# Performance work log

Hardware: AMD Instinct MI355X
Metric: run time of the kernel (lower is better)

Reference implementation:

```python
import jax, jax.numpy as jnp
import numpy as np

N_HEAD = 16
HEAD_DIM = 64

def setup_inputs() -> dict:
    key = jax.random.key(0)
    k1, k2, k3 = jax.random.split(key, 3)
    B, S, D = 4, 2048, 1024
    x = jax.random.normal(k1, (B, S, D), dtype=jnp.float32)
    mask = jnp.tril(jnp.ones((S, S), dtype=bool))[None, None]  # (1,1,S,S) causal
    w_attn = jax.random.normal(k2, (D, 3 * D), dtype=jnp.float32) * (1.0 / np.sqrt(D))
    b_attn = jnp.zeros((3 * D,), dtype=jnp.float32)
    w_proj = jax.random.normal(k3, (D, D), dtype=jnp.float32) * (1.0 / np.sqrt(D))
    b_proj = jnp.zeros((D,), dtype=jnp.float32)
    return {"x": x, "mask": mask, "w_attn": w_attn, "b_attn": b_attn,
            "w_proj": w_proj, "b_proj": b_proj}

def reference(x, mask, w_attn, b_attn, w_proj, b_proj):
    B, S, D = x.shape
    H, hd = N_HEAD, HEAD_DIM
    qkv = x @ w_attn + b_attn                      # (B,S,3D)
    q, k, v = jnp.split(qkv, 3, axis=-1)
    q = q.reshape(B, S, H, hd).transpose(0, 2, 1, 3)  # (B,H,S,hd)
    k = k.reshape(B, S, H, hd).transpose(0, 2, 1, 3)
    v = v.reshape(B, S, H, hd).transpose(0, 2, 1, 3)
    scores = jnp.einsum('bhqd,bhkd->bhqk', q, k) / jnp.sqrt(jnp.float32(hd))
    scores = jnp.where(mask, scores, jnp.float32(-1e10))
    weights = jax.nn.softmax(scores, axis=-1)      # dropout is identity (deterministic=True)
    attn = jnp.einsum('bhqk,bhkd->bhqd', weights, v)
    attn = attn.transpose(0, 2, 1, 3).reshape(B, S, D)
    return attn @ w_proj + b_proj
```

## Files before the change

### kernel.cpp

```cpp
#include <hip/hip_runtime.h>
#include <hip/hip_bf16.h>
#include <stdint.h>


typedef uint16_t u16;
typedef __bf16 bf16x8 __attribute__((ext_vector_type(8)));
typedef __bf16 bf16x4 __attribute__((ext_vector_type(4)));
typedef float f32x4 __attribute__((ext_vector_type(4)));

#define S_LEN 2048
#define DMODEL 1024
#define NHEAD 16
#define HDIM 64
#define MTOT 8192
#define NQKV 3072

__device__ __forceinline__ u16 f2bf(float f) {
    union { float f; uint32_t u; } v; v.f = f;
    uint32_t u = v.u;
    return (u16)((u + 0x7fffu + ((u >> 16) & 1u)) >> 16);
}

__device__ __forceinline__ void async_load16(const void* g, void* l) {
    __builtin_amdgcn_global_load_lds(
        (__attribute__((address_space(1))) void*)g,
        (__attribute__((address_space(3))) void*)l,
        16, 0, 0);
}

__global__ void convert_x_kernel(const float4* __restrict__ in, ushort4* __restrict__ out, int n4) {
    int i = blockIdx.x * 256 + threadIdx.x;
    if (i < n4) {
        float4 f = in[i];
        ushort4 o;
        o.x = f2bf(f.x); o.y = f2bf(f.y); o.z = f2bf(f.z); o.w = f2bf(f.w);
        out[i] = o;
    }
}

__global__ void transpose_bf16_kernel(const float* __restrict__ in, u16* __restrict__ out, int R, int C) {
    __shared__ float tile[64][65];
    int r0 = blockIdx.y * 64, c0 = blockIdx.x * 64;
    #pragma unroll
    for (int i = 0; i < 16; ++i) {
        int idx = threadIdx.x + i * 256;
        int r = idx >> 6, c = idx & 63;
        tile[r][c] = in[(size_t)(r0 + r) * C + c0 + c];
    }
    __syncthreads();
    #pragma unroll
    for (int i = 0; i < 16; ++i) {
        int idx = threadIdx.x + i * 256;
        int c = idx >> 6, r = idx & 63;
        out[(size_t)(c0 + c) * R + r0 + r] = f2bf(tile[r][c]);
    }
}

__global__ void transpose_v_kernel(const u16* __restrict__ qkv, u16* __restrict__ vt) {
    __shared__ u16 tile[64 * 66];
    const int tid = threadIdx.x;
    const int stile = blockIdx.x, bh = blockIdx.y;
    const int b = bh >> 4, h = bh & 15;
    const u16* src = qkv + ((size_t)b * S_LEN + stile * 64) * NQKV + 2 * DMODEL + h * HDIM;
    #pragma unroll
    for (int it = 0; it < 2; ++it) {
        int item = it * 256 + tid;
        int s = item >> 3, d0 = (item & 7) * 8;
        bf16x8 v = *(const bf16x8*)(src + (size_t)s * NQKV + d0);
        const u16* vu = (const u16*)&v;
        #pragma unroll
        for (int j = 0; j < 8; ++j) tile[(d0 + j) * 66 + s] = vu[j];
    }
    __syncthreads();
    #pragma unroll
    for (int it = 0; it < 2; ++it) {
        int item = it * 256 + tid;
        int d = item >> 3, s0 = (item & 7) * 8;
        union { u16 u[8]; uint4 v; } pk;
        #pragma unroll
        for (int j = 0; j < 8; ++j) pk.u[j] = tile[d * 66 + s0 + j];
        *(uint4*)(vt + ((size_t)bh * 64 + d) * S_LEN + stile * 64 + s0) = pk.v;
    }
}

template<bool OUT_BF16>
__global__ __launch_bounds__(256, 2) void gemm_bt(
    const u16* __restrict__ A, const u16* __restrict__ Bt,
    const float* __restrict__ bias, void* __restrict__ C,
    int M, int N, int K)
{
    __shared__ __attribute__((aligned(16))) u16 As[128 * 32];
    __shared__ __attribute__((aligned(16))) u16 Bs[128 * 32];
    const int tid = threadIdx.x;
    const int wave = tid >> 6, lane = tid & 63;
    const int l15 = lane & 15, q4 = lane >> 4;
    const int wm = wave >> 1, wn = wave & 1;
    const int m0 = blockIdx.x * 128, n0 = blockIdx.y * 128;

    f32x4 acc[4][4] = {};

    const int srow = lane >> 2;
    const int scol = (lane & 3) * 8;

    for (int k0 = 0; k0 < K; k0 += 32) {
        #pragma unroll
        for (int q = 0; q < 2; ++q) {
            int r = wave * 32 + q * 16 + srow;
            async_load16(A  + (size_t)(m0 + r) * K + k0 + scol, As + (wave * 32 + q * 16) * 32);
            async_load16(Bt + (size_t)(n0 + r) * K + k0 + scol, Bs + (wave * 32 + q * 16) * 32);
        }
        __syncthreads();

        bf16x8 af[4], bfr[4];
        #pragma unroll
        for (int t = 0; t < 4; ++t) {
            af[t]  = *(const bf16x8*)(As + (wm * 64 + t * 16 + l15) * 32 + q4 * 8);
            bfr[t] = *(const bf16x8*)(Bs + (wn * 64 + t * 16 + l15) * 32 + q4 * 8);
        }
        #pragma unroll
        for (int tm = 0; tm < 4; ++tm)
            #pragma unroll
            for (int tn = 0; tn < 4; ++tn)
                acc[tm][tn] = __builtin_amdgcn_mfma_f32_16x16x32_bf16(af[tm], bfr[tn], acc[tm][tn], 0, 0, 0);
        __syncthreads();
    }

    #pragma unroll
    for (int tm = 0; tm < 4; ++tm) {
        int row = m0 + wm * 64 + tm * 16 + q4 * 4;
        #pragma unroll
        for (int tn = 0; tn < 4; ++tn) {
            int col = n0 + wn * 64 + tn * 16 + l15;
            float bv = bias[col];
            #pragma unroll
            for (int r2 = 0; r2 < 4; ++r2) {
                float v = acc[tm][tn][r2] + bv;
                if (OUT_BF16) ((u16*)C)[(size_t)(row + r2) * N + col] = f2bf(v);
                else          ((float*)C)[(size_t)(row + r2) * N + col] = v;
            }
        }
    }
}

#define PW_LD 68
__global__ __launch_bounds__(256, 3) void attn_kernel(
    const u16* __restrict__ qkv, const u16* __restrict__ vt, u16* __restrict__ out)
{
    __shared__ __attribute__((aligned(16))) u16 Ks[2][64 * 64];
    __shared__ __attribute__((aligned(16))) u16 Vs[2][64 * 64];
    __shared__ __attribute__((aligned(16))) __bf16 Pw[4][32 * PW_LD];

    const int tid = threadIdx.x;
    const int w = tid >> 6, lane = tid & 63;
    const int l15 = lane & 15, q4 = lane >> 4;
    const int qt = (int)gridDim.x - 1 - (int)blockIdx.x;
    const int bh = blockIdx.y;
    const int b = bh >> 4, h = bh & 15;
    const size_t base = (size_t)b * S_LEN;

    bf16x8 qf[2][2];
    #pragma unroll
    for (int mh = 0; mh < 2; ++mh) {
        int qrow = qt * 128 + mh * 64 + w * 16 + l15;
        #pragma unroll
        for (int kc = 0; kc < 2; ++kc) {
            bf16x8 raw = *(const bf16x8*)(qkv + (base + qrow) * (size_t)NQKV + h * HDIM + kc * 32 + q4 * 8);
            bf16x8 sc;
            #pragma unroll
            for (int j = 0; j < 8; ++j) sc[j] = (__bf16)((float)raw[j] * 0.125f);
            qf[mh][kc] = sc;
        }
    }

    bf16x8 onesv;
    #pragma unroll
    for (int j = 0; j < 8; ++j) onesv[j] = (__bf16)1.0f;

    f32x4 o0[4] = {}, o1[4] = {};
    f32x4 l0 = {}, l1 = {};

    const int srow8 = lane >> 3, schunk = lane & 7;

    #define STAGE(kt_, buf_)                                                          \
        _Pragma("unroll")                                                             \
        for (int q = 0; q < 2; ++q) {                                                 \
            int rloc = w * 16 + q * 8 + srow8;                                        \
            int sc = ((schunk ^ (rloc & 7)) * 8);                                     \
            async_load16(qkv + (base + (kt_) * 64 + rloc) * (size_t)NQKV + DMODEL     \
                             + h * HDIM + sc,                                         \
                         &Ks[buf_][(w * 16 + q * 8) * 64]);                           \
            async_load16(vt + ((size_t)bh * 64 + rloc) * S_LEN + (kt_) * 64 + sc,     \
                         &Vs[buf_][(w * 16 + q * 8) * 64]);                           \
        }

    STAGE(0, 0);

    const int ktdiag = 2 * qt;
    for (int kt = 0; kt <= ktdiag; ++kt) {
        const int buf = kt & 1;
        __syncthreads();
        STAGE(kt + 1, buf ^ 1);

        f32x4 s0[4] = {}, s1[4] = {};
        #pragma unroll
        for (int nt = 0; nt < 4; ++nt) {
            int n = nt * 16 + l15;
            #pragma unroll
            for (int kc = 0; kc < 2; ++kc) {
                int ch = (((kc * 4 + q4) ^ (n & 7)) * 8);
                bf16x8 kf = *(const bf16x8*)(&Ks[buf][n * 64 + ch]);
                s0[nt] = __builtin_amdgcn_mfma_f32_16x16x32_bf16(qf[0][kc], kf, s0[nt], 0, 0, 0);
                s1[nt] = __builtin_amdgcn_mfma_f32_16x16x32_bf16(qf[1][kc], kf, s1[nt], 0, 0, 0);
            }
        }

        if (kt == ktdiag) {
            #pragma unroll
            for (int nt = 0; nt < 4; ++nt) {
                int col = nt * 16 + l15;
                #pragma unroll
                for (int r = 0; r < 4; ++r) {
                    int row = w * 16 + q4 * 4 + r;
                    if (col > row) s0[nt][r] = -1e30f;
                }
            }
        }

        #pragma unroll
        for (int nt = 0; nt < 4; ++nt)
            #pragma unroll
            for (int r = 0; r < 4; ++r) {
                Pw[w][(q4 * 4 + r) * PW_LD + nt * 16 + l15]        = (__bf16)__expf(s0[nt][r]);
                Pw[w][(16 + q4 * 4 + r) * PW_LD + nt * 16 + l15]   = (__bf16)__expf(s1[nt][r]);
            }

        bf16x8 pf0[2], pf1[2];
        #pragma unroll
        for (int kc = 0; kc < 2; ++kc) {
            bf16x4 a0 = *(const bf16x4*)(&Pw[w][l15 * PW_LD + kc * 32 + q4 * 8]);
            bf16x4 b0 = *(const bf16x4*)(&Pw[w][l15 * PW_LD + kc * 32 + q4 * 8 + 4]);
            bf16x4 a1 = *(const bf16x4*)(&Pw[w][(16 + l15) * PW_LD + kc * 32 + q4 * 8]);
            bf16x4 b1 = *(const bf16x4*)(&Pw[w][(16 + l15) * PW_LD + kc * 32 + q4 * 8 + 4]);
            bf16x8 p0, p1;
            #pragma unroll
            for (int j = 0; j < 4; ++j) {
                p0[j] = a0[j]; p0[4 + j] = b0[j];
                p1[j] = a1[j]; p1[4 + j] = b1[j];
            }
            pf0[kc] = p0; pf1[kc] = p1;
        }

        #pragma unroll
        for (int nt = 0; nt < 4; ++nt) {
            int n = nt * 16 + l15;
            #pragma unroll
            for (int kc = 0; kc < 2; ++kc) {
                int ch = (((kc * 4 + q4) ^ (n & 7)) * 8);
                bf16x8 vf = *(const bf16x8*)(&Vs[buf][n * 64 + ch]);
                o0[nt] = __builtin_amdgcn_mfma_f32_16x16x32_bf16(pf0[kc], vf, o0[nt], 0, 0, 0);
                o1[nt] = __builtin_amdgcn_mfma_f32_16x16x32_bf16(pf1[kc], vf, o1[nt], 0, 0, 0);
            }
        }
        #pragma unroll
        for (int kc = 0; kc < 2; ++kc) {
            l0 = __builtin_amdgcn_mfma_f32_16x16x32_bf16(pf0[kc], onesv, l0, 0, 0, 0);
            l1 = __builtin_amdgcn_mfma_f32_16x16x32_bf16(pf1[kc], onesv, l1, 0, 0, 0);
        }
    }

    {
        const int buf = (ktdiag + 1) & 1;
        __syncthreads();

        f32x4 s1[4] = {};
        #pragma unroll
        for (int nt = 0; nt < 4; ++nt) {
            int n = nt * 16 + l15;
            #pragma unroll
            for (int kc = 0; kc < 2; ++kc) {
                int ch = (((kc * 4 + q4) ^ (n & 7)) * 8);
                bf16x8 kf = *(const bf16x8*)(&Ks[buf][n * 64 + ch]);
                s1[nt] = __builtin_amdgcn_mfma_f32_16x16x32_bf16(qf[1][kc], kf, s1[nt], 0, 0, 0);
            }
        }
        #pragma unroll
        for (int nt = 0; nt < 4; ++nt) {
            int col = nt * 16 + l15;
            #pragma unroll
            for (int r = 0; r < 4; ++r) {
                int row = w * 16 + q4 * 4 + r;
                if (col > row) s1[nt][r] = -1e30f;
                Pw[w][(16 + q4 * 4 + r) * PW_LD + nt * 16 + l15] = (__bf16)__expf(s1[nt][r]);
            }
        }
        bf16x8 pf1[2];
        #pragma unroll
        for (int kc = 0; kc < 2; ++kc) {
            bf16x4 a1 = *(const bf16x4*)(&Pw[w][(16 + l15) * PW_LD + kc * 32 + q4 * 8]);
            bf16x4 b1 = *(const bf16x4*)(&Pw[w][(16 + l15) * PW_LD + kc * 32 + q4 * 8 + 4]);
            bf16x8 p1;
            #pragma unroll
            for (int j = 0; j < 4; ++j) { p1[j] = a1[j]; p1[4 + j] = b1[j]; }
            pf1[kc] = p1;
        }
        #pragma unroll
        for (int nt = 0; nt < 4; ++nt) {
            int n = nt * 16 + l15;
            #pragma unroll
            for (int kc = 0; kc < 2; ++kc) {
                int ch = (((kc * 4 + q4) ^ (n & 7)) * 8);
                bf16x8 vf = *(const bf16x8*)(&Vs[buf][n * 64 + ch]);
                o1[nt] = __builtin_amdgcn_mfma_f32_16x16x32_bf16(pf1[kc], vf, o1[nt], 0, 0, 0);
            }
        }
        #pragma unroll
        for (int kc = 0; kc < 2; ++kc)
            l1 = __builtin_amdgcn_mfma_f32_16x16x32_bf16(pf1[kc], onesv, l1, 0, 0, 0);
    }

    __bf16* outb = (__bf16*)out;
    #pragma unroll
    for (int r = 0; r < 4; ++r) {
        float inv0 = 1.0f / l0[r], inv1 = 1.0f / l1[r];
        int row0 = qt * 128 + w * 16 + q4 * 4 + r;
        int row1 = row0 + 64;
        #pragma unroll
        for (int nt = 0; nt < 4; ++nt) {
            int col = h * HDIM + nt * 16 + l15;
            outb[(base + row0) * (size_t)DMODEL + col] = (__bf16)(o0[nt][r] * inv0);
            outb[(base + row1) * (size_t)DMODEL + col] = (__bf16)(o1[nt][r] * inv1);
        }
    }
}

extern "C" void kernel_launch(void* const* d_in, const int* in_sizes, int n_in,
                              void* d_out, int out_size, void* d_ws, size_t ws_size,
                              hipStream_t stream) {
    const float* x      = (const float*)d_in[0];
    const float* w_attn = (const float*)d_in[2];
    const float* b_attn = (const float*)d_in[3];
    const float* w_proj = (const float*)d_in[4];
    const float* b_proj = (const float*)d_in[5];

    u16* xb   = (u16*)d_ws;
    u16* wat  = xb  + (size_t)MTOT * DMODEL;
    u16* wpt  = wat + (size_t)NQKV * DMODEL;
    u16* qkv  = wpt + (size_t)DMODEL * DMODEL;
    u16* attn = qkv + (size_t)MTOT * NQKV;
    u16* vt   = xb;

    convert_x_kernel<<<(MTOT * DMODEL / 4 + 255) / 256, 256, 0, stream>>>(
        (const float4*)x, (ushort4*)xb, MTOT * DMODEL / 4);
    transpose_bf16_kernel<<<dim3(NQKV / 64, DMODEL / 64), 256, 0, stream>>>(w_attn, wat, DMODEL, NQKV);
    transpose_bf16_kernel<<<dim3(DMODEL / 64, DMODEL / 64), 256, 0, stream>>>(w_proj, wpt, DMODEL, DMODEL);

    gemm_bt<true><<<dim3(MTOT / 128, NQKV / 128), 256, 0, stream>>>(
        xb, wat, b_attn, (void*)qkv, MTOT, NQKV, DMODEL);

    transpose_v_kernel<<<dim3(S_LEN / 64, 4 * NHEAD), 256, 0, stream>>>(qkv, vt);

    attn_kernel<<<dim3(S_LEN / 128, 4 * NHEAD), 256, 0, stream>>>(qkv, vt, attn);

    gemm_bt<false><<<dim3(MTOT / 128, DMODEL / 128), 256, 0, stream>>>(
        attn, wpt, b_proj, d_out, MTOT, DMODEL, DMODEL);
}
```

Measured before the change: 306.6 us.

## Compute transposed scores to keep P in registers; swizzle GEMM block order

The attention kernel now computes S^T = K·Q^T, so each lane's exp'd probabilities already sit in the B-operand layout of a 16x16x16 MFMA. That lets P·V (as V^T·P^T) run directly from registers and drops the per-wave LDS round trip for P along with its shared memory. Less LDS use allows raising launch bounds to 4 blocks per CU, at the cost of twice as many smaller MFMAs and more register pressure. Separately, the GEMM remaps block IDs into panels of 8 M-tiles so neighbouring blocks share input tiles in L2.

```diff
diff --git a/kernel.cpp b/kernel.cpp
--- a/kernel.cpp
+++ b/kernel.cpp
@@ -6,6 +6,7 @@
 typedef uint16_t u16;
 typedef __bf16 bf16x8 __attribute__((ext_vector_type(8)));
 typedef __bf16 bf16x4 __attribute__((ext_vector_type(4)));
+typedef short s16x4 __attribute__((ext_vector_type(4)));
 typedef float f32x4 __attribute__((ext_vector_type(4)));
 
 #define S_LEN 2048
@@ -19,6 +20,14 @@
     union { float f; uint32_t u; } v; v.f = f;
     uint32_t u = v.u;
     return (u16)((u + 0x7fffu + ((u >> 16) & 1u)) >> 16);
+}
+
+__device__ __forceinline__ s16x4 bits4(bf16x4 v) {
+    union { bf16x4 b; s16x4 s; } u; u.b = v; return u.s;
+}
+
+__device__ __forceinline__ f32x4 mfma16(bf16x4 a, bf16x4 b, f32x4 c) {
+    return __builtin_amdgcn_mfma_f32_16x16x16bf16_1k(bits4(a), bits4(b), c, 0, 0, 0);
 }
 
 __device__ __forceinline__ void async_load16(const void* g, void* l) {
@@ -95,7 +104,15 @@
     const int wave = tid >> 6, lane = tid & 63;
     const int l15 = lane & 15, q4 = lane >> 4;
     const int wm = wave >> 1, wn = wave & 1;
-    const int m0 = blockIdx.x * 128, n0 = blockIdx.y * 128;
+
+    const int gx = gridDim.x, gy = gridDim.y;
+    int bid = (int)blockIdx.y * gx + (int)blockIdx.x;
+    const int PANEL = 8;
+    int panel = bid / (PANEL * gy);
+    int within = bid - panel * (PANEL * gy);
+    int mb = panel * PANEL + (within % PANEL);
+    int nb = within / PANEL;
+    const int m0 = mb * 128, n0 = nb * 128;
 
     f32x4 acc[4][4] = {};
 
@@ -142,13 +159,11 @@
     }
 }
 
-#define PW_LD 68
-__global__ __launch_bounds__(256, 3) void attn_kernel(
+__global__ __launch_bounds__(256, 4) void attn_kernel(
     const u16* __restrict__ qkv, const u16* __restrict__ vt, u16* __restrict__ out)
 {
     __shared__ __attribute__((aligned(16))) u16 Ks[2][64 * 64];
     __shared__ __attribute__((aligned(16))) u16 Vs[2][64 * 64];
-    __shared__ __attribute__((aligned(16))) __bf16 Pw[4][32 * PW_LD];
 
     const int tid = threadIdx.x;
     const int w = tid >> 6, lane = tid & 63;
@@ -172,12 +187,12 @@
         }
     }
 
-    bf16x8 onesv;
-    #pragma unroll
-    for (int j = 0; j < 8; ++j) onesv[j] = (__bf16)1.0f;
+    bf16x4 ones4;
+    #pragma unroll
+    for (int j = 0; j < 4; ++j) ones4[j] = (__bf16)1.0f;
 
     f32x4 o0[4] = {}, o1[4] = {};
-    f32x4 l0 = {}, l1 = {};
+    f32x4 la0 = {}, la1 = {};
 
     const int srow8 = lane >> 3, schunk = lane & 7;
 
@@ -201,7 +216,7 @@
         __syncthreads();
         STAGE(kt + 1, buf ^ 1);
 
-        f32x4 s0[4] = {}, s1[4] = {};
+        f32x4 st0[4] = {}, st1[4] = {};
         #pragma unroll
         for (int nt = 0; nt < 4; ++nt) {
             int n = nt * 16 + l15;
@@ -209,62 +224,44 @@
             for (int kc = 0; kc < 2; ++kc) {
                 int ch = (((kc * 4 + q4) ^ (n & 7)) * 8);
                 bf16x8 kf = *(const bf16x8*)(&Ks[buf][n * 64 + ch]);
-                s0[nt] = __builtin_amdgcn_mfma_f32_16x16x32_bf16(qf[0][kc], kf, s0[nt], 0, 0, 0);
-                s1[nt] = __builtin_amdgcn_mfma_f32_16x16x32_bf16(qf[1][kc], kf, s1[nt], 0, 0, 0);
+                st0[nt] = __builtin_amdgcn_mfma_f32_16x16x32_bf16(kf, qf[0][kc], st0[nt], 0, 0, 0);
+                st1[nt] = __builtin_amdgcn_mfma_f32_16x16x32_bf16(kf, qf[1][kc], st1[nt], 0, 0, 0);
             }
         }
 
         if (kt == ktdiag) {
             #pragma unroll
             for (int nt = 0; nt < 4; ++nt) {
-                int col = nt * 16 + l15;
                 #pragma unroll
                 for (int r = 0; r < 4; ++r) {
-                    int row = w * 16 + q4 * 4 + r;
-                    if (col > row) s0[nt][r] = -1e30f;
+                    int keyl = nt * 16 + q4 * 4 + r;
+                    if (keyl > w * 16 + l15) st0[nt][r] = -1e30f;
                 }
             }
         }
 
-        #pragma unroll
-        for (int nt = 0; nt < 4; ++nt)
+        bf16x4 pb0[4], pb1[4];
+        #pragma unroll
+        for (int nt = 0; nt < 4; ++nt) {
             #pragma unroll
             for (int r = 0; r < 4; ++r) {
-                Pw[w][(q4 * 4 + r) * PW_LD + nt * 16 + l15]        = (__bf16)__expf(s0[nt][r]);
-                Pw[w][(16 + q4 * 4 + r) * PW_LD + nt * 16 + l15]   = (__bf16)__expf(s1[nt][r]);
-            }
-
-        bf16x8 pf0[2], pf1[2];
-        #pragma unroll
-        for (int kc = 0; kc < 2; ++kc) {
-            bf16x4 a0 = *(const bf16x4*)(&Pw[w][l15 * PW_LD + kc * 32 + q4 * 8]);
-            bf16x4 b0 = *(const bf16x4*)(&Pw[w][l15 * PW_LD + kc * 32 + q4 * 8 + 4]);
-            bf16x4 a1 = *(const bf16x4*)(&Pw[w][(16 + l15) * PW_LD + kc * 32 + q4 * 8]);
-            bf16x4 b1 = *(const bf16x4*)(&Pw[w][(16 + l15) * PW_LD + kc * 32 + q4 * 8 + 4]);
-            bf16x8 p0, p1;
-            #pragma unroll
-            for (int j = 0; j < 4; ++j) {
-                p0[j] = a0[j]; p0[4 + j] = b0[j];
-                p1[j] = a1[j]; p1[4 + j] = b1[j];
-            }
-            pf0[kc] = p0; pf1[kc] = p1;
-        }
-
-        #pragma unroll
-        for (int nt = 0; nt < 4; ++nt) {
-            int n = nt * 16 + l15;
-            #pragma unroll
-            for (int kc = 0; kc < 2; ++kc) {
-                int ch = (((kc * 4 + q4) ^ (n & 7)) * 8);
-                bf16x8 vf = *(const bf16x8*)(&Vs[buf][n * 64 + ch]);
-                o0[nt] = __builtin_amdgcn_mfma_f32_16x16x32_bf16(pf0[kc], vf, o0[nt], 0, 0, 0);
-                o1[nt] = __builtin_amdgcn_mfma_f32_16x16x32_bf16(pf1[kc], vf, o1[nt], 0, 0, 0);
-            }
-        }
-        #pragma unroll
-        for (int kc = 0; kc < 2; ++kc) {
-            l0 = __builtin_amdgcn_mfma_f32_16x16x32_bf16(pf0[kc], onesv, l0, 0, 0, 0);
-            l1 = __builtin_amdgcn_mfma_f32_16x16x32_bf16(pf1[kc], onesv, l1, 0, 0, 0);
+                pb0[nt][r] = (__bf16)__expf(st0[nt][r]);
+                pb1[nt][r] = (__bf16)__expf(st1[nt][r]);
+            }
+        }
+
+        #pragma unroll
+        for (int nt = 0; nt < 4; ++nt) {
+            #pragma unroll
+            for (int mt = 0; mt < 4; ++mt) {
+                int row = mt * 16 + l15;
+                int ch = (nt * 2 + (q4 >> 1)) ^ (row & 7);
+                bf16x4 vf = *(const bf16x4*)(&Vs[buf][row * 64 + ch * 8 + (q4 & 1) * 4]);
+                o0[mt] = mfma16(vf, pb0[nt], o0[mt]);
+                o1[mt] = mfma16(vf, pb1[nt], o1[mt]);
+            }
+            la0 = mfma16(ones4, pb0[nt], la0);
+            la1 = mfma16(ones4, pb1[nt], la1);
         }
     }
 
@@ -272,7 +269,7 @@
         const int buf = (ktdiag + 1) & 1;
         __syncthreads();
 
-        f32x4 s1[4] = {};
+        f32x4 st1[4] = {};
         #pragma unroll
         for (int nt = 0; nt < 4; ++nt) {
             int n = nt * 16 + l15;
@@ -280,55 +277,43 @@
             for (int kc = 0; kc < 2; ++kc) {
                 int ch = (((kc * 4 + q4) ^ (n & 7)) * 8);
                 bf16x8 kf = *(const bf16x8*)(&Ks[buf][n * 64 + ch]);
-                s1[nt] = __builtin_amdgcn_mfma_f32_16x16x32_bf16(qf[1][kc], kf, s1[nt], 0, 0, 0);
-            }
-        }
-        #pragma unroll
-        for (int nt = 0; nt < 4; ++nt) {
-            int col = nt * 16 + l15;
+                st1[nt] = __builtin_amdgcn_mfma_f32_16x16x32_bf16(kf, qf[1][kc], st1[nt], 0, 0, 0);
+            }
+        }
+        bf16x4 pb1[4];
+        #pragma unroll
+        for (int nt = 0; nt < 4; ++nt) {
             #pragma unroll
             for (int r = 0; r < 4; ++r) {
-                int row = w * 16 + q4 * 4 + r;
-                if (col > row) s1[nt][r] = -1e30f;
-                Pw[w][(16 + q4 * 4 + r) * PW_LD + nt * 16 + l15] = (__bf16)__expf(s1[nt][r]);
-            }
-        }
-        bf16x8 pf1[2];
-        #pragma unroll
-        for (int kc = 0; kc < 2; ++kc) {
-            bf16x4 a1 = *(const bf16x4*)(&Pw[w][(16 + l15) * PW_LD + kc * 32 + q4 * 8]);
-            bf16x4 b1 = *(const bf16x4*)(&Pw[w][(16 + l15) * PW_LD + kc * 32 + q4 * 8 + 4]);
-            bf16x8 p1;
-            #pragma unroll
-            for (int j = 0; j < 4; ++j) { p1[j] = a1[j]; p1[4 + j] = b1[j]; }
-            pf1[kc] = p1;
-        }
-        #pragma unroll
-        for (int nt = 0; nt < 4; ++nt) {
-            int n = nt * 16 + l15;
-            #pragma unroll
-            for (int kc = 0; kc < 2; ++kc) {
-                int ch = (((kc * 4 + q4) ^ (n & 7)) * 8);
-                bf16x8 vf = *(const bf16x8*)(&Vs[buf][n * 64 + ch]);
-                o1[nt] = __builtin_amdgcn_mfma_f32_16x16x32_bf16(pf1[kc], vf, o1[nt], 0, 0, 0);
-            }
-        }
-        #pragma unroll
-        for (int kc = 0; kc < 2; ++kc)
-            l1 = __builtin_amdgcn_mfma_f32_16x16x32_bf16(pf1[kc], onesv, l1, 0, 0, 0);
+                int keyl = nt * 16 + q4 * 4 + r;
+                float s = (keyl > w * 16 + l15) ? -1e30f : st1[nt][r];
+                pb1[nt][r] = (__bf16)__expf(s);
+            }
+        }
+        #pragma unroll
+        for (int nt = 0; nt < 4; ++nt) {
+            #pragma unroll
+            for (int mt = 0; mt < 4; ++mt) {
+                int row = mt * 16 + l15;
+                int ch = (nt * 2 + (q4 >> 1)) ^ (row & 7);
+                bf16x4 vf = *(const bf16x4*)(&Vs[buf][row * 64 + ch * 8 + (q4 & 1) * 4]);
+                o1[mt] = mfma16(vf, pb1[nt], o1[mt]);
+            }
+            la1 = mfma16(ones4, pb1[nt], la1);
+        }
     }
 
     __bf16* outb = (__bf16*)out;
-    #pragma unroll
-    for (int r = 0; r < 4; ++r) {
-        float inv0 = 1.0f / l0[r], inv1 = 1.0f / l1[r];
-        int row0 = qt * 128 + w * 16 + q4 * 4 + r;
-        int row1 = row0 + 64;
-        #pragma unroll
-        for (int nt = 0; nt < 4; ++nt) {
-            int col = h * HDIM + nt * 16 + l15;
-            outb[(base + row0) * (size_t)DMODEL + col] = (__bf16)(o0[nt][r] * inv0);
-            outb[(base + row1) * (size_t)DMODEL + col] = (__bf16)(o1[nt][r] * inv1);
+    float inv0 = 1.0f / la0[0], inv1 = 1.0f / la1[0];
+    int row0 = qt * 128 + w * 16 + l15;
+    int row1 = row0 + 64;
+    #pragma unroll
+    for (int mt = 0; mt < 4; ++mt) {
+        #pragma unroll
+        for (int r = 0; r < 4; ++r) {
+            int col = h * HDIM + mt * 16 + q4 * 4 + r;
+            outb[(base + row0) * (size_t)DMODEL + col] = (__bf16)(o0[mt][r] * inv0);
+            outb[(base + row1) * (size_t)DMODEL + col] = (__bf16)(o1[mt][r] * inv1);
         }
     }
 }
```

Measured after the change: 301.4 us. No clear change (-1.7%).
